# Kernel optimization log

Hardware: AMD Instinct MI355X
Metric: run time of the kernel (lower is better)

## Reference

```python
import jax, jax.numpy as jnp
import numpy as np

H, C, PQ, PV = 12, 16, 4, 8   # heads, c_hidden, qk points, v points
CS, CZ = 384, 128
INF, EPS = 1e5, 1e-8


def quat_to_rot(q):
    w, x, y, z = q[..., 0], q[..., 1], q[..., 2], q[..., 3]
    r = jnp.stack([
        1 - 2 * (y * y + z * z), 2 * (x * y - w * z), 2 * (x * z + w * y),
        2 * (x * y + w * z), 1 - 2 * (x * x + z * z), 2 * (y * z - w * x),
        2 * (x * z - w * y), 2 * (y * z + w * x), 1 - 2 * (x * x + y * y)],
        axis=-1)
    return r.reshape(q.shape[:-1] + (3, 3))


def setup_inputs() -> dict:
    key = jax.random.key(0)
    ks = jax.random.split(key, 20)
    B, N = 1, 768
    s = jax.random.normal(ks[0], (B, N, CS), jnp.float32)
    z = jax.random.normal(ks[1], (B, N, N, CZ), jnp.float32)
    quat = jax.random.normal(ks[2], (B, N, 4), jnp.float32)
    quat = quat / jnp.linalg.norm(quat, axis=-1, keepdims=True)
    rot = quat_to_rot(quat)
    trans = 10.0 * jax.random.normal(ks[3], (B, N, 3), jnp.float32)
    mask = jnp.ones((B, N), jnp.float32)
    ss = jax.random.uniform(ks[4], (B, N, N), jnp.float32)
    sc = 0.02
    W_q = sc * jax.random.normal(ks[5], (CS, H * C), jnp.float32)
    b_q = jnp.zeros((H * C,), jnp.float32)
    W_kv = sc * jax.random.normal(ks[6], (CS, 2 * H * C), jnp.float32)
    b_kv = jnp.zeros((2 * H * C,), jnp.float32)
    W_qp = sc * jax.random.normal(ks[7], (CS, H * PQ * 3), jnp.float32)
    b_qp = jnp.zeros((H * PQ * 3,), jnp.float32)
    W_kvp = sc * jax.random.normal(ks[8], (CS, H * (PQ + PV) * 3), jnp.float32)
    b_kvp = jnp.zeros((H * (PQ + PV) * 3,), jnp.float32)
    W_b = sc * jax.random.normal(ks[9], (CZ, H), jnp.float32)
    b_b = jnp.zeros((H,), jnp.float32)
    head_weights = 0.1 * jax.random.normal(ks[10], (H,), jnp.float32)
    cdim = H * (CZ + C + PV * 4)
    W_out = sc * jax.random.normal(ks[11], (cdim, CS), jnp.float32)
    b_out = jnp.zeros((CS,), jnp.float32)
    return dict(s=s, z=z, rot=rot, trans=trans, mask=mask, ss=ss,
                W_q=W_q, b_q=b_q, W_kv=W_kv, b_kv=b_kv, W_qp=W_qp, b_qp=b_qp,
                W_kvp=W_kvp, b_kvp=b_kvp, W_b=W_b, b_b=b_b,
                head_weights=head_weights, W_out=W_out, b_out=b_out)


def reference(s, z, rot, trans, mask, ss, W_q, b_q, W_kv, b_kv, W_qp, b_qp,
              W_kvp, b_kvp, W_b, b_b, head_weights, W_out, b_out):
    B, N, _ = s.shape
    # scalar q/k/v  [B,N,H,C]
    q = (s @ W_q + b_q).reshape(B, N, H, C)
    kv = (s @ W_kv + b_kv).reshape(B, N, H, 2 * C)
    k, v = kv[..., :C], kv[..., C:]
    # point q/k/v: linear output is [x_all, y_all, z_all] -> stack on last dim
    qp = s @ W_qp + b_qp                                  # [B,N,H*PQ*3]
    qp = jnp.stack(jnp.split(qp, 3, axis=-1), axis=-1)    # [B,N,H*PQ,3] local
    qp = jnp.einsum('bnxy,bnpy->bnpx', rot, qp) + trans[:, :, None]
    qp = qp.reshape(B, N, H, PQ, 3)                       # global frame
    kvp = s @ W_kvp + b_kvp
    kvp = jnp.stack(jnp.split(kvp, 3, axis=-1), axis=-1)  # [B,N,H*(PQ+PV),3]
    kvp = jnp.einsum('bnxy,bnpy->bnpx', rot, kvp) + trans[:, :, None]
    kvp = kvp.reshape(B, N, H, PQ + PV, 3)
    kp, vp = kvp[..., :PQ, :], kvp[..., PQ:, :]
    # scalar attention logits + pair bias
    b = z @ W_b + b_b                                     # [B,N,N,H]
    a = jnp.einsum('bihc,bjhc->bhij', q, k) * np.sqrt(1.0 / (3 * C))
    a = a + np.sqrt(1.0 / 3) * jnp.transpose(b, (0, 3, 1, 2))
    # point-distance attention
    diff = qp[:, :, None] - kp[:, None]                   # [B,N,N,H,PQ,3]
    d2 = jnp.sum(diff * diff, axis=-1)                    # [B,N,N,H,PQ]
    hw = jax.nn.softplus(head_weights) * np.sqrt(1.0 / (3 * (PQ * 9.0 / 2)))
    pt = -0.5 * jnp.sum(d2 * hw[None, None, None, :, None], axis=-1)  # [B,N,N,H]
    a = a + jnp.transpose(pt, (0, 3, 1, 2))
    sq_mask = INF * (mask[:, :, None] * mask[:, None, :] - 1.0)
    a = a + sq_mask[:, None]
    # weighted softmax (ss_usage='multiply', t_ss=1): weights = exp(ss) - 0.99
    weights = jnp.exp(ss) - 0.99                          # [B,N,N]
    e = jnp.exp(a - jnp.max(a, axis=-1, keepdims=True))
    we = e * weights[:, None]
    a = we / jnp.sum(we, axis=-1, keepdims=True)          # [B,H,N,N]
    # outputs
    o = jnp.einsum('bhij,bjhc->bihc', a, v).reshape(B, N, H * C)
    o_pt = jnp.einsum('bhij,bjhpc->bihpc', a, vp)         # [B,N,H,PV,3] global
    o_pt = jnp.einsum('bnyx,bnhpy->bnhpx', rot, o_pt - trans[:, :, None, None])
    o_pt_norm = jnp.sqrt(jnp.sum(o_pt ** 2, axis=-1) + EPS).reshape(B, N, H * PV)
    o_pt = o_pt.reshape(B, N, H * PV, 3)
    o_pair = jnp.einsum('bhij,bijc->bihc', a, z).reshape(B, N, H * CZ)
    cat = jnp.concatenate(
        [o, o_pt[..., 0], o_pt[..., 1], o_pt[..., 2], o_pt_norm, o_pair], axis=-1)
    return cat @ W_out + b_out
```

## Files before the change

### kernel.cpp

```cpp
#include <hip/hip_runtime.h>
#include <math.h>

#define NN 768
#define CSD 384
#define HD 12
#define CD 16
#define PQD 4
#define PVD 8
#define CZD 128
#define CATD 2112

#define OFF_Q      0u
#define OFF_K      147456u
#define OFF_V      294912u
#define OFF_QP     442368u
#define OFF_KP     552960u
#define OFF_VP     663552u
#define OFF_RAW    884736u
#define OFF_B      1327104u
#define OFF_A      8404992u
#define OFF_CAT    15482880u

__device__ __forceinline__ float wcol_val(const float* Wq, const float* Wkv,
                                          const float* Wqp, const float* Wkvp,
                                          int k, int col) {
  if (col < 192) return Wq[k*192 + col];
  if (col < 576) return Wkv[k*384 + (col-192)];
  if (col < 720) return Wqp[k*144 + (col-576)];
  return Wkvp[k*432 + (col-720)];
}
__device__ __forceinline__ float bias_val(const float* bq, const float* bkv,
                                          const float* bqp, const float* bkvp, int col) {
  if (col < 192) return bq[col];
  if (col < 576) return bkv[col-192];
  if (col < 720) return bqp[col-576];
  return bkvp[col-720];
}

__global__ __launch_bounds__(256) void k_proj(const float* __restrict__ s,
    const float* __restrict__ Wq, const float* __restrict__ bq,
    const float* __restrict__ Wkv, const float* __restrict__ bkv,
    const float* __restrict__ Wqp, const float* __restrict__ bqp,
    const float* __restrict__ Wkvp, const float* __restrict__ bkvp,
    float* __restrict__ ws) {
  __shared__ float At[64*17];
  __shared__ float Bt[16*64];
  int t = threadIdx.x;
  int c0 = blockIdx.x * 64;
  int r0 = blockIdx.y * 64;
  float acc[4][4] = {};
  int cc = t & 15, rr = t >> 4;
  for (int kt = 0; kt < CSD; kt += 16) {
    int ka = t & 15, mb = t >> 4;
#pragma unroll
    for (int p = 0; p < 4; ++p) {
      int m = mb + p*16;
      At[m*17 + ka] = s[(r0+m)*CSD + kt + ka];
    }
    int cb = t & 63, kb = t >> 6;
#pragma unroll
    for (int p = 0; p < 4; ++p) {
      int kk = kb + p*4;
      Bt[kk*64 + cb] = wcol_val(Wq,Wkv,Wqp,Wkvp, kt+kk, c0+cb);
    }
    __syncthreads();
#pragma unroll
    for (int k = 0; k < 16; ++k) {
      float a0 = At[(rr*4+0)*17 + k];
      float a1 = At[(rr*4+1)*17 + k];
      float a2 = At[(rr*4+2)*17 + k];
      float a3 = At[(rr*4+3)*17 + k];
      float4 b4 = *(const float4*)&Bt[k*64 + cc*4];
      acc[0][0] = fmaf(a0,b4.x,acc[0][0]); acc[0][1] = fmaf(a0,b4.y,acc[0][1]);
      acc[0][2] = fmaf(a0,b4.z,acc[0][2]); acc[0][3] = fmaf(a0,b4.w,acc[0][3]);
      acc[1][0] = fmaf(a1,b4.x,acc[1][0]); acc[1][1] = fmaf(a1,b4.y,acc[1][1]);
      acc[1][2] = fmaf(a1,b4.z,acc[1][2]); acc[1][3] = fmaf(a1,b4.w,acc[1][3]);
      acc[2][0] = fmaf(a2,b4.x,acc[2][0]); acc[2][1] = fmaf(a2,b4.y,acc[2][1]);
      acc[2][2] = fmaf(a2,b4.z,acc[2][2]); acc[2][3] = fmaf(a2,b4.w,acc[2][3]);
      acc[3][0] = fmaf(a3,b4.x,acc[3][0]); acc[3][1] = fmaf(a3,b4.y,acc[3][1]);
      acc[3][2] = fmaf(a3,b4.z,acc[3][2]); acc[3][3] = fmaf(a3,b4.w,acc[3][3]);
    }
    __syncthreads();
  }
  float* qbuf = ws + OFF_Q; float* kbuf = ws + OFF_K; float* vbuf = ws + OFF_V;
  float* raw  = ws + OFF_RAW;
#pragma unroll
  for (int jj = 0; jj < 4; ++jj) {
    int col = c0 + cc*4 + jj;
    float bv = bias_val(bq,bkv,bqp,bkvp,col);
#pragma unroll
    for (int ii = 0; ii < 4; ++ii) {
      int row = r0 + rr*4 + ii;
      float val = acc[ii][jj] + bv;
      if (col < 192) {
        int h = col >> 4, c = col & 15;
        qbuf[(h*NN + row)*CD + c] = val;
      } else if (col < 576) {
        int u = col - 192; int h = u >> 5; int c2 = u & 31;
        if (c2 < 16) kbuf[(h*NN+row)*CD + c2] = val;
        else         vbuf[(h*NN+row)*CD + (c2-16)] = val;
      } else {
        raw[row*576 + (col-576)] = val;
      }
    }
  }
}

__global__ __launch_bounds__(256) void k_points(const float* __restrict__ rot,
    const float* __restrict__ trans, const float* __restrict__ bout,
    float* __restrict__ out, float* __restrict__ ws) {
  int bx = blockIdx.x;
  if (bx >= 576) {
    int idx = (bx - 576)*256 + threadIdx.x;
    out[idx] = bout[idx % CSD];
    return;
  }
  int tg = bx*256 + threadIdx.x;
  int n = tg / 192, pidx = tg % 192;
  const float* raw = ws + OFF_RAW + n*576;
  float v0, v1, v2;
  if (pidx < 48) { v0 = raw[pidx]; v1 = raw[48+pidx]; v2 = raw[96+pidx]; }
  else { int pp = pidx-48; v0 = raw[144+pp]; v1 = raw[288+pp]; v2 = raw[432+pp]; }
  const float* R = rot + n*9; const float* T = trans + n*3;
  float g0 = R[0]*v0 + R[1]*v1 + R[2]*v2 + T[0];
  float g1 = R[3]*v0 + R[4]*v1 + R[5]*v2 + T[1];
  float g2 = R[6]*v0 + R[7]*v1 + R[8]*v2 + T[2];
  if (pidx < 48) {
    int h = pidx >> 2, p = pidx & 3;
    float* qp = ws + OFF_QP + ((h*NN + n)*PQD + p)*3;
    qp[0]=g0; qp[1]=g1; qp[2]=g2;
  } else {
    int pp = pidx - 48; int h = pp/12; int q12 = pp - 12*h;
    if (q12 < 4) { float* kp = ws + OFF_KP + ((h*NN+n)*PQD + q12)*3; kp[0]=g0; kp[1]=g1; kp[2]=g2; }
    else         { float* vp = ws + OFF_VP + ((h*NN+n)*PVD + (q12-4))*3; vp[0]=g0; vp[1]=g1; vp[2]=g2; }
  }
}

#define BR 128
#define BPAD 130
__global__ __launch_bounds__(256) void k_bias(const float* __restrict__ z,
    const float* __restrict__ Wb, const float* __restrict__ bb, float* __restrict__ ws) {
  __shared__ float zt[BR*BPAD];
  int t = threadIdx.x;
  int q = t & 15;
  int rg = t >> 4;
  float wbr[8][12];
#pragma unroll
  for (int cc = 0; cc < 8; ++cc) {
    const float* wp = Wb + (q*8 + cc)*HD;
#pragma unroll
    for (int h = 0; h < 12; ++h) wbr[cc][h] = wp[h];
  }
  const int b3=(q>>3)&1, b2=(q>>2)&1, b1=(q>>1)&1, b0=q&1;
  const int hmine = 6*b3 + 3*b2 + (b1 ? 2 : b0);
  const bool writer = !(b1 && b0);
  const float bbh = bb[hmine];

  const int rowbase = blockIdx.x * 1152;
  float* bmat = ws + OFF_B;
  const float s2 = 0.57735026918962576f;

  for (int T = 0; T < 9; ++T) {
    int r0 = rowbase + T*BR;
#pragma unroll 4
    for (int it = 0; it < 16; ++it) {
      int g = it*256 + t;
      int row = g >> 5, f4 = g & 31;
      float4 v = *(const float4*)(z + (size_t)(r0+row)*CZD + f4*4);
      float* d = &zt[row*BPAD + f4*4];
      *(float2*)(d)   = make_float2(v.x, v.y);
      *(float2*)(d+2) = make_float2(v.z, v.w);
    }
    __syncthreads();
#pragma unroll 2
    for (int ps = 0; ps < 8; ++ps) {
      int row = ps*16 + rg;
      const float* zr = &zt[row*BPAD + q*8];
      float2 z01 = *(const float2*)(zr);
      float2 z23 = *(const float2*)(zr+2);
      float2 z45 = *(const float2*)(zr+4);
      float2 z67 = *(const float2*)(zr+6);
      float acc[12];
#pragma unroll
      for (int h = 0; h < 12; ++h) {
        float a = z01.x*wbr[0][h];
        a = fmaf(z01.y, wbr[1][h], a);
        a = fmaf(z23.x, wbr[2][h], a);
        a = fmaf(z23.y, wbr[3][h], a);
        a = fmaf(z45.x, wbr[4][h], a);
        a = fmaf(z45.y, wbr[5][h], a);
        a = fmaf(z67.x, wbr[6][h], a);
        a = fmaf(z67.y, wbr[7][h], a);
        acc[h] = a;
      }
      float na[6];
#pragma unroll
      for (int m = 0; m < 6; ++m) {
        float keep = b3 ? acc[m+6] : acc[m];
        float give = b3 ? acc[m]   : acc[m+6];
        na[m] = keep + __shfl_xor(give, 8);
      }
      float nb[3];
#pragma unroll
      for (int m = 0; m < 3; ++m) {
        float keep = b2 ? na[m+3] : na[m];
        float give = b2 ? na[m]   : na[m+3];
        nb[m] = keep + __shfl_xor(give, 4);
      }
      float k0 = b1 ? nb[2] : nb[0];
      float g0v = b1 ? nb[0] : nb[2];
      float k1 = b1 ? 0.f   : nb[1];
      float g1v = b1 ? nb[1] : 0.f;
      float c0v = k0 + __shfl_xor(g0v, 2);
      float c1v = k1 + __shfl_xor(g1v, 2);
      float k2 = b1 ? c0v : (b0 ? c1v : c0v);
      float g2v = b1 ? c0v : (b0 ? c0v : c1v);
      float d0 = k2 + __shfl_xor(g2v, 1);
      if (writer) {
        int r = r0 + row;
        int i = r / NN;
        int j = r - i*NN;
        bmat[((size_t)i*HD + hmine)*NN + j] = s2*(d0 + bbh);
      }
    }
    __syncthreads();
  }
}

__global__ __launch_bounds__(256) void k_attn(
    const float* __restrict__ mask, const float* __restrict__ ss,
    const float* __restrict__ hwts, float* __restrict__ ws) {
  int h = blockIdx.x, i = blockIdx.y;
  int t = threadIdx.x;
  __shared__ float qsm[16];
  __shared__ float qpsm[12];
  __shared__ float wred[8];
  const float* qbuf = ws + OFF_Q; const float* kbuf = ws + OFF_K;
  const float* qp   = ws + OFF_QP; const float* kp  = ws + OFF_KP;
  const float* bmat = ws + OFF_B;
  float* abuf = ws + OFF_A;
  if (t < 16) qsm[t] = qbuf[(h*NN+i)*CD + t];
  else if (t < 28) qpsm[t-16] = qp[(h*NN+i)*12 + (t-16)];
  __syncthreads();
  float coef = -0.5f * 0.13608276348795434f * log1pf(__expf(hwts[h]));
  float mi = mask[i];
  const float s1 = 0.14433756729740643f;
  float l3[3], ss3[3];
#pragma unroll
  for (int jj = 0; jj < 3; ++jj) {
    int j = t + jj*256;
    const float4* kb = (const float4*)(kbuf + (h*NN+j)*CD);
    float dot = 0.f;
#pragma unroll
    for (int u = 0; u < 4; ++u) {
      float4 kv = kb[u];
      dot = fmaf(qsm[u*4+0], kv.x, dot);
      dot = fmaf(qsm[u*4+1], kv.y, dot);
      dot = fmaf(qsm[u*4+2], kv.z, dot);
      dot = fmaf(qsm[u*4+3], kv.w, dot);
    }
    const float4* kpb = (const float4*)(kp + (h*NN+j)*12);
    float pts = 0.f;
#pragma unroll
    for (int u = 0; u < 3; ++u) {
      float4 kpv = kpb[u];
      float d;
      d = qpsm[u*4+0]-kpv.x; pts = fmaf(d,d,pts);
      d = qpsm[u*4+1]-kpv.y; pts = fmaf(d,d,pts);
      d = qpsm[u*4+2]-kpv.z; pts = fmaf(d,d,pts);
      d = qpsm[u*4+3]-kpv.w; pts = fmaf(d,d,pts);
    }
    float bterm = bmat[((size_t)i*HD + h)*NN + j];
    float lg = fmaf(dot, s1, bterm) + coef*pts + 100000.0f*(mi*mask[j] - 1.0f);
    l3[jj] = lg; ss3[jj] = ss[i*NN + j];
  }
  float mx = fmaxf(l3[0], fmaxf(l3[1], l3[2]));
#pragma unroll
  for (int off = 32; off >= 1; off >>= 1) mx = fmaxf(mx, __shfl_xor(mx, off));
  if ((t & 63) == 0) wred[t>>6] = mx;
  __syncthreads();
  mx = fmaxf(fmaxf(wred[0],wred[1]), fmaxf(wred[2],wred[3]));
  float e3[3]; float sum = 0.f;
#pragma unroll
  for (int jj = 0; jj < 3; ++jj) {
    e3[jj] = __expf(l3[jj]-mx) * (__expf(ss3[jj]) - 0.99f);
    sum += e3[jj];
  }
#pragma unroll
  for (int off = 32; off >= 1; off >>= 1) sum += __shfl_xor(sum, off);
  if ((t & 63) == 0) wred[4 + (t>>6)] = sum;
  __syncthreads();
  sum = (wred[4]+wred[5]) + (wred[6]+wred[7]);
  float inv = 1.0f / sum;
#pragma unroll
  for (int jj = 0; jj < 3; ++jj)
    abuf[((size_t)h*NN + i)*NN + t + jj*256] = e3[jj]*inv;
}

__global__ __launch_bounds__(256) void k_out_v(
    const float* __restrict__ rot, const float* __restrict__ trans, float* __restrict__ ws) {
  int h = blockIdx.x;
  int i = blockIdx.y*4 + (threadIdx.x >> 6);
  int lane = threadIdx.x & 63;
  const float* abuf = ws + OFF_A; const float* vbuf = ws + OFF_V; const float* vpbuf = ws + OFF_VP;
  float* cat = ws + OFF_CAT;
  const float* arow = abuf + ((size_t)h*NN + i)*NN;
  float acc = 0.f;
  if (lane < 40) {
    const float* ptr; int stride;
    if (lane < 16) { ptr = vbuf + (size_t)(h*NN)*CD + lane; stride = CD; }
    else           { ptr = vpbuf + (size_t)(h*NN)*24 + (lane-16); stride = 24; }
    for (int j = 0; j < NN; j += 4) {
      float4 a4 = *(const float4*)(arow + j);
      float x0 = ptr[0];
      float x1 = ptr[stride];
      float x2 = ptr[2*stride];
      float x3 = ptr[3*stride];
      ptr += 4*stride;
      acc = fmaf(a4.x, x0, acc);
      acc = fmaf(a4.y, x1, acc);
      acc = fmaf(a4.z, x2, acc);
      acc = fmaf(a4.w, x3, acc);
    }
  }
  if (lane < 16) {
    cat[(size_t)i*CATD + h*CD + lane] = acc;
  } else if (lane < 40) {
    int pv = lane - 16; int p = pv/3; int x = pv - 3*p;
    int base = 16 + p*3;
    float g0 = __shfl(acc, base+0);
    float g1 = __shfl(acc, base+1);
    float g2 = __shfl(acc, base+2);
    float v0 = g0 - trans[i*3+0];
    float v1 = g1 - trans[i*3+1];
    float v2 = g2 - trans[i*3+2];
    float loc = rot[i*9 + 0*3 + x]*v0 + rot[i*9 + 1*3 + x]*v1 + rot[i*9 + 2*3 + x]*v2;
    cat[(size_t)i*CATD + 192 + x*96 + h*PVD + p] = loc;
    float sq = loc*loc;
    float n2 = __shfl(sq, base+0) + __shfl(sq, base+1) + __shfl(sq, base+2);
    if (x == 0) cat[(size_t)i*CATD + 480 + h*PVD + p] = sqrtf(n2 + 1e-8f);
  }
}

__global__ __launch_bounds__(256) void k_out_pair(const float* __restrict__ z, float* __restrict__ ws) {
  __shared__ float a_sm[HD*NN];
  __shared__ float4 psm[2][HD][32];
  int i = blockIdx.x;
  int t = threadIdx.x;
  const float* abuf = ws + OFF_A;
  float* cat = ws + OFF_CAT;
  for (int h = 0; h < HD; ++h) {
    if (t < 192)
      *(float4*)&a_sm[h*NN + t*4] = *(const float4*)(abuf + ((size_t)h*NN + i)*NN + t*4);
  }
  __syncthreads();
  int c4 = t & 31, jc = t >> 5;
  const float* zbase = z + ((size_t)i*NN + (size_t)jc*96)*CZD + c4*4;
  float4 acc[12];
#pragma unroll
  for (int h = 0; h < 12; ++h) acc[h] = make_float4(0.f,0.f,0.f,0.f);
  for (int jj = 0; jj < 96; jj += 4) {
    float4 z0 = *(const float4*)(zbase + (size_t)(jj+0)*CZD);
    float4 z1 = *(const float4*)(zbase + (size_t)(jj+1)*CZD);
    float4 z2 = *(const float4*)(zbase + (size_t)(jj+2)*CZD);
    float4 z3 = *(const float4*)(zbase + (size_t)(jj+3)*CZD);
    int j0 = jc*96 + jj;
#pragma unroll
    for (int h = 0; h < 12; ++h) {
      float4 av = *(const float4*)&a_sm[h*NN + j0];
      acc[h].x = fmaf(av.x, z0.x, acc[h].x); acc[h].y = fmaf(av.x, z0.y, acc[h].y);
      acc[h].z = fmaf(av.x, z0.z, acc[h].z); acc[h].w = fmaf(av.x, z0.w, acc[h].w);
      acc[h].x = fmaf(av.y, z1.x, acc[h].x); acc[h].y = fmaf(av.y, z1.y, acc[h].y);
      acc[h].z = fmaf(av.y, z1.z, acc[h].z); acc[h].w = fmaf(av.y, z1.w, acc[h].w);
      acc[h].x = fmaf(av.z, z2.x, acc[h].x); acc[h].y = fmaf(av.z, z2.y, acc[h].y);
      acc[h].z = fmaf(av.z, z2.z, acc[h].z); acc[h].w = fmaf(av.z, z2.w, acc[h].w);
      acc[h].x = fmaf(av.w, z3.x, acc[h].x); acc[h].y = fmaf(av.w, z3.y, acc[h].y);
      acc[h].z = fmaf(av.w, z3.z, acc[h].z); acc[h].w = fmaf(av.w, z3.w, acc[h].w);
    }
  }
  int wv = t >> 6, ln = t & 63;
#pragma unroll
  for (int h = 0; h < 12; ++h) {
    acc[h].x += __shfl_down(acc[h].x, 32);
    acc[h].y += __shfl_down(acc[h].y, 32);
    acc[h].z += __shfl_down(acc[h].z, 32);
    acc[h].w += __shfl_down(acc[h].w, 32);
  }
  if (wv >= 2 && ln < 32) {
#pragma unroll
    for (int h = 0; h < 12; ++h) psm[wv-2][h][ln] = acc[h];
  }
  __syncthreads();
  if (wv < 2 && ln < 32) {
#pragma unroll
    for (int h = 0; h < 12; ++h) {
      float4 p = psm[wv][h][ln];
      acc[h].x += p.x; acc[h].y += p.y; acc[h].z += p.z; acc[h].w += p.w;
      psm[wv][h][ln] = acc[h];
    }
  }
  __syncthreads();
  for (int o = t; o < 384; o += 256) {
    int h = o >> 5, cc = o & 31;
    float4 s0 = psm[0][h][cc], s1 = psm[1][h][cc];
    float4 r;
    r.x = s0.x + s1.x;
    r.y = s0.y + s1.y;
    r.z = s0.z + s1.z;
    r.w = s0.w + s1.w;
    *(float4*)&cat[(size_t)i*CATD + 576 + h*CZD + cc*4] = r;
  }
}

__global__ __launch_bounds__(256) void k_final(const float* __restrict__ Wout,
    float* __restrict__ out, const float* __restrict__ ws) {
  __shared__ float At[64*17];
  __shared__ float Bt[16*64];
  const float* cat = ws + OFF_CAT;
  int t = threadIdx.x;
  int c0 = blockIdx.x*64, r0 = blockIdx.y*64;
  int kstart = blockIdx.z*528;
  float acc[4][4] = {};
  int cc = t & 15, rr = t >> 4;
  for (int kt = 0; kt < 528; kt += 16) {
    int ka = t & 15, mb = t >> 4;
#pragma unroll
    for (int p = 0; p < 4; ++p) {
      int m = mb + p*16;
      At[m*17 + ka] = cat[(size_t)(r0+m)*CATD + kstart + kt + ka];
    }
    int cb = t & 63, kb = t >> 6;
#pragma unroll
    for (int p = 0; p < 4; ++p) {
      int kk = kb + p*4;
      Bt[kk*64 + cb] = Wout[(size_t)(kstart+kt+kk)*CSD + c0 + cb];
    }
    __syncthreads();
#pragma unroll
    for (int k = 0; k < 16; ++k) {
      float a0 = At[(rr*4+0)*17 + k];
      float a1 = At[(rr*4+1)*17 + k];
      float a2 = At[(rr*4+2)*17 + k];
      float a3 = At[(rr*4+3)*17 + k];
      float4 b4 = *(const float4*)&Bt[k*64 + cc*4];
      acc[0][0] = fmaf(a0,b4.x,acc[0][0]); acc[0][1] = fmaf(a0,b4.y,acc[0][1]);
      acc[0][2] = fmaf(a0,b4.z,acc[0][2]); acc[0][3] = fmaf(a0,b4.w,acc[0][3]);
      acc[1][0] = fmaf(a1,b4.x,acc[1][0]); acc[1][1] = fmaf(a1,b4.y,acc[1][1]);
      acc[1][2] = fmaf(a1,b4.z,acc[1][2]); acc[1][3] = fmaf(a1,b4.w,acc[1][3]);
      acc[2][0] = fmaf(a2,b4.x,acc[2][0]); acc[2][1] = fmaf(a2,b4.y,acc[2][1]);
      acc[2][2] = fmaf(a2,b4.z,acc[2][2]); acc[2][3] = fmaf(a2,b4.w,acc[2][3]);
      acc[3][0] = fmaf(a3,b4.x,acc[3][0]); acc[3][1] = fmaf(a3,b4.y,acc[3][1]);
      acc[3][2] = fmaf(a3,b4.z,acc[3][2]); acc[3][3] = fmaf(a3,b4.w,acc[3][3]);
    }
    __syncthreads();
  }
#pragma unroll
  for (int ii = 0; ii < 4; ++ii)
#pragma unroll
    for (int jj = 0; jj < 4; ++jj)
      atomicAdd(&out[(size_t)(r0+rr*4+ii)*CSD + c0 + cc*4 + jj], acc[ii][jj]);
}

extern "C" void kernel_launch(void* const* d_in, const int* in_sizes, int n_in,
                              void* d_out, int out_size, void* d_ws, size_t ws_size,
                              hipStream_t stream) {
  const float* s    = (const float*)d_in[0];
  const float* z    = (const float*)d_in[1];
  const float* rot  = (const float*)d_in[2];
  const float* trans= (const float*)d_in[3];
  const float* mask = (const float*)d_in[4];
  const float* ss   = (const float*)d_in[5];
  const float* Wq   = (const float*)d_in[6];
  const float* bq   = (const float*)d_in[7];
  const float* Wkv  = (const float*)d_in[8];
  const float* bkv  = (const float*)d_in[9];
  const float* Wqp  = (const float*)d_in[10];
  const float* bqp  = (const float*)d_in[11];
  const float* Wkvp = (const float*)d_in[12];
  const float* bkvp = (const float*)d_in[13];
  const float* Wb   = (const float*)d_in[14];
  const float* bb   = (const float*)d_in[15];
  const float* hw   = (const float*)d_in[16];
  const float* Wout = (const float*)d_in[17];
  const float* bout = (const float*)d_in[18];
  float* ws  = (float*)d_ws;
  float* out = (float*)d_out;

  hipLaunchKernelGGL(k_proj, dim3(18,12), dim3(256), 0, stream,
                     s, Wq,bq, Wkv,bkv, Wqp,bqp, Wkvp,bkvp, ws);
  hipLaunchKernelGGL(k_points, dim3(1728), dim3(256), 0, stream, rot, trans, bout, out, ws);
  hipLaunchKernelGGL(k_bias, dim3(512), dim3(256), 0, stream, z, Wb, bb, ws);
  hipLaunchKernelGGL(k_attn, dim3(12,768), dim3(256), 0, stream, mask, ss, hw, ws);
  hipLaunchKernelGGL(k_out_v, dim3(12,192), dim3(256), 0, stream, rot, trans, ws);
  hipLaunchKernelGGL(k_out_pair, dim3(768), dim3(256), 0, stream, z, ws);
  hipLaunchKernelGGL(k_final, dim3(6,12,4), dim3(256), 0, stream, Wout, out, ws);
}
```

Before: 825.1 us.

## Fuse attention softmax, value aggregation and pair aggregation into one kernel

Replaces the separate attention, value-output and pair-output kernels with a single per-row kernel that computes softmax weights for all heads into shared memory and consumes them directly. This removes writing and re-reading the full H×N×N attention matrix in global memory and two kernel launches. In exchange, the attention phase runs with only one block per row and loops over heads serially with barriers, reducing parallelism for that stage.

```diff
diff --git a/kernel.cpp b/kernel.cpp
--- a/kernel.cpp
+++ b/kernel.cpp
@@ -227,133 +227,143 @@
   }
 }
 
-__global__ __launch_bounds__(256) void k_attn(
+__global__ __launch_bounds__(256) void k_fused(
+    const float* __restrict__ z,
+    const float* __restrict__ rot, const float* __restrict__ trans,
     const float* __restrict__ mask, const float* __restrict__ ss,
     const float* __restrict__ hwts, float* __restrict__ ws) {
-  int h = blockIdx.x, i = blockIdx.y;
+  __shared__ float a_sm[HD*NN];
+  __shared__ float4 psm[2][HD][32];
+  __shared__ float wred[8];
+  int i = blockIdx.x;
   int t = threadIdx.x;
-  __shared__ float qsm[16];
-  __shared__ float qpsm[12];
-  __shared__ float wred[8];
   const float* qbuf = ws + OFF_Q; const float* kbuf = ws + OFF_K;
   const float* qp   = ws + OFF_QP; const float* kp  = ws + OFF_KP;
+  const float* vbuf = ws + OFF_V;  const float* vpbuf = ws + OFF_VP;
   const float* bmat = ws + OFF_B;
-  float* abuf = ws + OFF_A;
-  if (t < 16) qsm[t] = qbuf[(h*NN+i)*CD + t];
-  else if (t < 28) qpsm[t-16] = qp[(h*NN+i)*12 + (t-16)];
-  __syncthreads();
-  float coef = -0.5f * 0.13608276348795434f * log1pf(__expf(hwts[h]));
+  float* cat = ws + OFF_CAT;
+  const float s1 = 0.14433756729740643f;
+
   float mi = mask[i];
-  const float s1 = 0.14433756729740643f;
-  float l3[3], ss3[3];
+  float msk3[3], ss3[3];
 #pragma unroll
   for (int jj = 0; jj < 3; ++jj) {
     int j = t + jj*256;
-    const float4* kb = (const float4*)(kbuf + (h*NN+j)*CD);
-    float dot = 0.f;
-#pragma unroll
-    for (int u = 0; u < 4; ++u) {
-      float4 kv = kb[u];
-      dot = fmaf(qsm[u*4+0], kv.x, dot);
-      dot = fmaf(qsm[u*4+1], kv.y, dot);
-      dot = fmaf(qsm[u*4+2], kv.z, dot);
-      dot = fmaf(qsm[u*4+3], kv.w, dot);
-    }
-    const float4* kpb = (const float4*)(kp + (h*NN+j)*12);
-    float pts = 0.f;
-#pragma unroll
-    for (int u = 0; u < 3; ++u) {
-      float4 kpv = kpb[u];
-      float d;
-      d = qpsm[u*4+0]-kpv.x; pts = fmaf(d,d,pts);
-      d = qpsm[u*4+1]-kpv.y; pts = fmaf(d,d,pts);
-      d = qpsm[u*4+2]-kpv.z; pts = fmaf(d,d,pts);
-      d = qpsm[u*4+3]-kpv.w; pts = fmaf(d,d,pts);
-    }
-    float bterm = bmat[((size_t)i*HD + h)*NN + j];
-    float lg = fmaf(dot, s1, bterm) + coef*pts + 100000.0f*(mi*mask[j] - 1.0f);
-    l3[jj] = lg; ss3[jj] = ss[i*NN + j];
-  }
-  float mx = fmaxf(l3[0], fmaxf(l3[1], l3[2]));
-#pragma unroll
-  for (int off = 32; off >= 1; off >>= 1) mx = fmaxf(mx, __shfl_xor(mx, off));
-  if ((t & 63) == 0) wred[t>>6] = mx;
+    msk3[jj] = 100000.0f*(mi*mask[j] - 1.0f);
+    ss3[jj]  = __expf(ss[i*NN + j]) - 0.99f;
+  }
+
+  for (int h = 0; h < HD; ++h) {
+    const float4* qv4 = (const float4*)(qbuf + (h*NN+i)*CD);
+    float4 q0 = qv4[0], q1 = qv4[1], q2 = qv4[2], q3 = qv4[3];
+    const float4* qp4 = (const float4*)(qp + (h*NN+i)*12);
+    float4 p0 = qp4[0], p1 = qp4[1], p2 = qp4[2];
+    float coef = -0.5f * 0.13608276348795434f * log1pf(__expf(hwts[h]));
+    float l3[3];
+#pragma unroll
+    for (int jj = 0; jj < 3; ++jj) {
+      int j = t + jj*256;
+      const float4* kb = (const float4*)(kbuf + (h*NN+j)*CD);
+      float dot = 0.f;
+      float4 kv;
+      kv = kb[0];
+      dot = fmaf(q0.x, kv.x, dot); dot = fmaf(q0.y, kv.y, dot);
+      dot = fmaf(q0.z, kv.z, dot); dot = fmaf(q0.w, kv.w, dot);
+      kv = kb[1];
+      dot = fmaf(q1.x, kv.x, dot); dot = fmaf(q1.y, kv.y, dot);
+      dot = fmaf(q1.z, kv.z, dot); dot = fmaf(q1.w, kv.w, dot);
+      kv = kb[2];
+      dot = fmaf(q2.x, kv.x, dot); dot = fmaf(q2.y, kv.y, dot);
+      dot = fmaf(q2.z, kv.z, dot); dot = fmaf(q2.w, kv.w, dot);
+      kv = kb[3];
+      dot = fmaf(q3.x, kv.x, dot); dot = fmaf(q3.y, kv.y, dot);
+      dot = fmaf(q3.z, kv.z, dot); dot = fmaf(q3.w, kv.w, dot);
+      const float4* kpb = (const float4*)(kp + (h*NN+j)*12);
+      float pts = 0.f; float d;
+      float4 kpv;
+      kpv = kpb[0];
+      d = p0.x-kpv.x; pts = fmaf(d,d,pts);
+      d = p0.y-kpv.y; pts = fmaf(d,d,pts);
+      d = p0.z-kpv.z; pts = fmaf(d,d,pts);
+      d = p0.w-kpv.w; pts = fmaf(d,d,pts);
+      kpv = kpb[1];
+      d = p1.x-kpv.x; pts = fmaf(d,d,pts);
+      d = p1.y-kpv.y; pts = fmaf(d,d,pts);
+      d = p1.z-kpv.z; pts = fmaf(d,d,pts);
+      d = p1.w-kpv.w; pts = fmaf(d,d,pts);
+      kpv = kpb[2];
+      d = p2.x-kpv.x; pts = fmaf(d,d,pts);
+      d = p2.y-kpv.y; pts = fmaf(d,d,pts);
+      d = p2.z-kpv.z; pts = fmaf(d,d,pts);
+      d = p2.w-kpv.w; pts = fmaf(d,d,pts);
+      float bterm = bmat[((size_t)i*HD + h)*NN + j];
+      l3[jj] = fmaf(dot, s1, bterm) + coef*pts + msk3[jj];
+    }
+    float mx = fmaxf(l3[0], fmaxf(l3[1], l3[2]));
+#pragma unroll
+    for (int off = 32; off >= 1; off >>= 1) mx = fmaxf(mx, __shfl_xor(mx, off));
+    if ((t & 63) == 0) wred[t>>6] = mx;
+    __syncthreads();
+    mx = fmaxf(fmaxf(wred[0],wred[1]), fmaxf(wred[2],wred[3]));
+    float e3[3]; float sum = 0.f;
+#pragma unroll
+    for (int jj = 0; jj < 3; ++jj) {
+      e3[jj] = __expf(l3[jj]-mx) * ss3[jj];
+      sum += e3[jj];
+    }
+#pragma unroll
+    for (int off = 32; off >= 1; off >>= 1) sum += __shfl_xor(sum, off);
+    if ((t & 63) == 0) wred[4 + (t>>6)] = sum;
+    __syncthreads();
+    sum = (wred[4]+wred[5]) + (wred[6]+wred[7]);
+    float inv = 1.0f / sum;
+#pragma unroll
+    for (int jj = 0; jj < 3; ++jj)
+      a_sm[h*NN + t + jj*256] = e3[jj]*inv;
+  }
   __syncthreads();
-  mx = fmaxf(fmaxf(wred[0],wred[1]), fmaxf(wred[2],wred[3]));
-  float e3[3]; float sum = 0.f;
-#pragma unroll
-  for (int jj = 0; jj < 3; ++jj) {
-    e3[jj] = __expf(l3[jj]-mx) * (__expf(ss3[jj]) - 0.99f);
-    sum += e3[jj];
-  }
-#pragma unroll
-  for (int off = 32; off >= 1; off >>= 1) sum += __shfl_xor(sum, off);
-  if ((t & 63) == 0) wred[4 + (t>>6)] = sum;
-  __syncthreads();
-  sum = (wred[4]+wred[5]) + (wred[6]+wred[7]);
-  float inv = 1.0f / sum;
-#pragma unroll
-  for (int jj = 0; jj < 3; ++jj)
-    abuf[((size_t)h*NN + i)*NN + t + jj*256] = e3[jj]*inv;
-}
-
-__global__ __launch_bounds__(256) void k_out_v(
-    const float* __restrict__ rot, const float* __restrict__ trans, float* __restrict__ ws) {
-  int h = blockIdx.x;
-  int i = blockIdx.y*4 + (threadIdx.x >> 6);
-  int lane = threadIdx.x & 63;
-  const float* abuf = ws + OFF_A; const float* vbuf = ws + OFF_V; const float* vpbuf = ws + OFF_VP;
-  float* cat = ws + OFF_CAT;
-  const float* arow = abuf + ((size_t)h*NN + i)*NN;
-  float acc = 0.f;
-  if (lane < 40) {
-    const float* ptr; int stride;
-    if (lane < 16) { ptr = vbuf + (size_t)(h*NN)*CD + lane; stride = CD; }
-    else           { ptr = vpbuf + (size_t)(h*NN)*24 + (lane-16); stride = 24; }
-    for (int j = 0; j < NN; j += 4) {
-      float4 a4 = *(const float4*)(arow + j);
-      float x0 = ptr[0];
-      float x1 = ptr[stride];
-      float x2 = ptr[2*stride];
-      float x3 = ptr[3*stride];
-      ptr += 4*stride;
-      acc = fmaf(a4.x, x0, acc);
-      acc = fmaf(a4.y, x1, acc);
-      acc = fmaf(a4.z, x2, acc);
-      acc = fmaf(a4.w, x3, acc);
-    }
-  }
-  if (lane < 16) {
-    cat[(size_t)i*CATD + h*CD + lane] = acc;
-  } else if (lane < 40) {
-    int pv = lane - 16; int p = pv/3; int x = pv - 3*p;
-    int base = 16 + p*3;
-    float g0 = __shfl(acc, base+0);
-    float g1 = __shfl(acc, base+1);
-    float g2 = __shfl(acc, base+2);
-    float v0 = g0 - trans[i*3+0];
-    float v1 = g1 - trans[i*3+1];
-    float v2 = g2 - trans[i*3+2];
-    float loc = rot[i*9 + 0*3 + x]*v0 + rot[i*9 + 1*3 + x]*v1 + rot[i*9 + 2*3 + x]*v2;
-    cat[(size_t)i*CATD + 192 + x*96 + h*PVD + p] = loc;
-    float sq = loc*loc;
-    float n2 = __shfl(sq, base+0) + __shfl(sq, base+1) + __shfl(sq, base+2);
-    if (x == 0) cat[(size_t)i*CATD + 480 + h*PVD + p] = sqrtf(n2 + 1e-8f);
-  }
-}
-
-__global__ __launch_bounds__(256) void k_out_pair(const float* __restrict__ z, float* __restrict__ ws) {
-  __shared__ float a_sm[HD*NN];
-  __shared__ float4 psm[2][HD][32];
-  int i = blockIdx.x;
-  int t = threadIdx.x;
-  const float* abuf = ws + OFF_A;
-  float* cat = ws + OFF_CAT;
-  for (int h = 0; h < HD; ++h) {
-    if (t < 192)
-      *(float4*)&a_sm[h*NN + t*4] = *(const float4*)(abuf + ((size_t)h*NN + i)*NN + t*4);
-  }
-  __syncthreads();
+
+  int wv = t >> 6, lane = t & 63;
+  for (int hh = 0; hh < 3; ++hh) {
+    int h = wv*3 + hh;
+    float acc = 0.f;
+    if (lane < 40) {
+      const float* ptr; int stride;
+      if (lane < 16) { ptr = vbuf + (size_t)(h*NN)*CD + lane; stride = CD; }
+      else           { ptr = vpbuf + (size_t)(h*NN)*24 + (lane-16); stride = 24; }
+      const float* arow = &a_sm[h*NN];
+      for (int j = 0; j < NN; j += 4) {
+        float4 a4 = *(const float4*)(arow + j);
+        float x0 = ptr[0];
+        float x1 = ptr[stride];
+        float x2 = ptr[2*stride];
+        float x3 = ptr[3*stride];
+        ptr += 4*stride;
+        acc = fmaf(a4.x, x0, acc);
+        acc = fmaf(a4.y, x1, acc);
+        acc = fmaf(a4.z, x2, acc);
+        acc = fmaf(a4.w, x3, acc);
+      }
+    }
+    if (lane < 16) {
+      cat[(size_t)i*CATD + h*CD + lane] = acc;
+    } else if (lane < 40) {
+      int pv = lane - 16; int p = pv/3; int x = pv - 3*p;
+      int base = 16 + p*3;
+      float g0 = __shfl(acc, base+0);
+      float g1 = __shfl(acc, base+1);
+      float g2 = __shfl(acc, base+2);
+      float v0 = g0 - trans[i*3+0];
+      float v1 = g1 - trans[i*3+1];
+      float v2 = g2 - trans[i*3+2];
+      float loc = rot[i*9 + 0*3 + x]*v0 + rot[i*9 + 1*3 + x]*v1 + rot[i*9 + 2*3 + x]*v2;
+      cat[(size_t)i*CATD + 192 + x*96 + h*PVD + p] = loc;
+      float sq = loc*loc;
+      float n2 = __shfl(sq, base+0) + __shfl(sq, base+1) + __shfl(sq, base+2);
+      if (x == 0) cat[(size_t)i*CATD + 480 + h*PVD + p] = sqrtf(n2 + 1e-8f);
+    }
+  }
+
   int c4 = t & 31, jc = t >> 5;
   const float* zbase = z + ((size_t)i*NN + (size_t)jc*96)*CZD + c4*4;
   float4 acc[12];
@@ -378,7 +388,7 @@
       acc[h].z = fmaf(av.w, z3.z, acc[h].z); acc[h].w = fmaf(av.w, z3.w, acc[h].w);
     }
   }
-  int wv = t >> 6, ln = t & 63;
+  int ln = t & 63;
 #pragma unroll
   for (int h = 0; h < 12; ++h) {
     acc[h].x += __shfl_down(acc[h].x, 32);
@@ -490,8 +500,6 @@
                      s, Wq,bq, Wkv,bkv, Wqp,bqp, Wkvp,bkvp, ws);
   hipLaunchKernelGGL(k_points, dim3(1728), dim3(256), 0, stream, rot, trans, bout, out, ws);
   hipLaunchKernelGGL(k_bias, dim3(512), dim3(256), 0, stream, z, Wb, bb, ws);
-  hipLaunchKernelGGL(k_attn, dim3(12,768), dim3(256), 0, stream, mask, ss, hw, ws);
-  hipLaunchKernelGGL(k_out_v, dim3(12,192), dim3(256), 0, stream, rot, trans, ws);
-  hipLaunchKernelGGL(k_out_pair, dim3(768), dim3(256), 0, stream, z, ws);
+  hipLaunchKernelGGL(k_fused, dim3(768), dim3(256), 0, stream, z, rot, trans, mask, ss, hw, ws);
   hipLaunchKernelGGL(k_final, dim3(6,12,4), dim3(256), 0, stream, Wout, out, ws);
 }
```

Measured after the change: 737.7 us. -10.6%, faster.
